# Performance work log

Measured on AMD Instinct MI355X. Metric: run time of the kernel, lower is better.

The kernel has to match this reference:

```python
import jax, jax.numpy as jnp
import numpy as np

T, NC, NT, D, H, LBL = 8, 512, 512, 256, 8, 3
NBF = 1419  # performer default: int(256 * ln(256))
EPS = 1e-4


def setup_inputs() -> dict:
    key = jax.random.key(0)
    ks = jax.random.split(key, 16)
    rn = lambda i, shape, sc=1.0: jax.random.normal(ks[i], shape, dtype=jnp.float32) * sc
    w = 1.0 / np.sqrt(D)
    return {
        'x_ctx': rn(0, (T, NC, D)),
        'label_train': rn(1, (T, NC, LBL)),
        'x_tgt': rn(2, (T, NT, D)),
        # task_encoder: 3-layer MLP (256+label_dim -> 256 -> 256 -> 256), ReLU
        'W1': rn(3, (D + LBL, D), 1.0 / np.sqrt(D + LBL)), 'b1': jnp.zeros((D,), jnp.float32),
        'W2': rn(4, (D, D), w), 'b2': jnp.zeros((D,), jnp.float32),
        'W3': rn(5, (D, D), w), 'b3': jnp.zeros((D,), jnp.float32),
        # per-head projections (8 distinct 256->256 Linears each for k/v/q)
        'Wk': rn(6, (H, D, D), w), 'bk': jnp.zeros((H, D), jnp.float32),
        'Wv': rn(7, (H, D, D), w), 'bv': jnp.zeros((H, D), jnp.float32),
        'Wq': rn(8, (H, D, D), w), 'bq': jnp.zeros((H, D), jnp.float32),
        # output head-merge projection (8*256 -> 256) and mu (256 -> 256)
        'Wo': rn(9, (H * D, D), 1.0 / np.sqrt(H * D)), 'bo': jnp.zeros((D,), jnp.float32),
        'Wmu': rn(10, (D, D), w), 'bmu': jnp.zeros((D,), jnp.float32),
        # FAVOR+ random projection matrix [nb_features, dim_head]
        'proj': rn(11, (NBF, D)),
    }


def _softmax_kernel(data, proj, is_query):
    # Performer FAVOR+ positive softmax-kernel features. data: [t,h,n,d]
    dn = D ** -0.25
    ratio = NBF ** -0.5
    dd = jnp.einsum('thnd,fd->thnf', data * dn, proj)          # [t,h,n,F]
    diag = 0.5 * jnp.sum(data * data, axis=-1) * (dn * dn)      # [t,h,n]
    if is_query:
        m = jnp.max(dd, axis=-1, keepdims=True)
    else:
        m = jnp.max(dd, axis=(-2, -1), keepdims=True)
    return ratio * (jnp.exp(dd - diag[..., None] - m) + EPS)


def reference(x_ctx, label_train, x_tgt, W1, b1, W2, b2, W3, b3,
              Wk, bk, Wv, bv, Wq, bq, Wo, bo, Wmu, bmu, proj):
    # task_encoder MLP on [x_ctx, label]
    h = jax.nn.relu(jnp.concatenate([x_ctx, label_train], axis=-1) @ W1 + b1)
    h = jax.nn.relu(h @ W2 + b2)
    cf = jax.nn.relu(h @ W3 + b3)                               # context_features [t,Nc,D]
    # per-head full-width projections: k from x_ctx, v from context_features, q from x_tgt
    k = jnp.einsum('tnd,hde->thne', x_ctx, Wk) + bk[None, :, None, :]
    v = jnp.einsum('tnd,hde->thne', cf, Wv) + bv[None, :, None, :]
    q = jnp.einsum('tnd,hde->thne', x_tgt, Wq) + bq[None, :, None, :]
    # non-causal Performer linear attention
    qp = _softmax_kernel(q, proj, True)                         # [t,h,Nt,F]
    kp = _softmax_kernel(k, proj, False)                        # [t,h,Nc,F]
    ksum = jnp.sum(kp, axis=-2)                                 # [t,h,F]
    d_inv = 1.0 / jnp.einsum('thnf,thf->thn', qp, ksum)         # [t,h,Nt]
    ctx = jnp.einsum('thnf,thne->thfe', kp, v)                  # [t,h,F,D]
    out = jnp.einsum('thnf,thfe,thn->thne', qp, ctx, d_inv)     # [t,h,Nt,D]
    # torch: permute(0,2,3,1).view(t,Nt,-1) -> head index fastest-varying
    out = jnp.transpose(out, (0, 2, 3, 1)).reshape(out.shape[0], out.shape[2], -1)
    rep = out @ Wo + bo                                         # [t,Nt,D]
    return rep @ Wmu + bmu                                      # mu / sample_features
```

## Files before the change

### kernel.cpp

```cpp
#include <hip/hip_runtime.h>
#include <hip/hip_bf16.h>

typedef __hip_bfloat16 bf16;
typedef __attribute__((ext_vector_type(8))) short short8;
typedef __attribute__((ext_vector_type(4))) float f32x4;
typedef __attribute__((ext_vector_type(4))) unsigned short us4;
#define DEV __device__ __forceinline__

static constexpr int T_ = 8, NC = 512, NT = 512, D_ = 256, H_ = 8, NBF = 1419;
static constexpr int FT32 = 46;
static constexpr float EPS_ = 1e-4f;
static constexpr float DN = 0.25f;
static constexpr float DIAG_SC = 0.03125f;

DEV float bf2f(unsigned short u) { return __uint_as_float(((unsigned)u) << 16); }
DEV float tofloat(bf16 x) { return __bfloat162float(x); }
DEV unsigned short f2bu(float x) { bf16 h = __float2bfloat16(x); return *(unsigned short*)&h; }

DEV float ldx(const void* p, long i, int isb) {
  if (isb) return bf2f(((const unsigned short*)p)[i]);
  return ((const float*)p)[i];
}
DEV void stx(void* p, long i, float v, int isb) {
  if (isb) ((bf16*)p)[i] = __float2bfloat16(v);
  else     ((float*)p)[i] = v;
}

DEV void async_copy16(const void* g, void* lds) {
  __builtin_amdgcn_global_load_lds(
      (const __attribute__((address_space(1))) unsigned int*)g,
      (__attribute__((address_space(3))) unsigned int*)lds, 16, 0, 0);
}

__global__ __launch_bounds__(256)
void detect_dtype(const void* __restrict__ x, int* __restrict__ flag)
{
  __shared__ int bad;
  if (threadIdx.x == 0) bad = 0;
  __syncthreads();
  int mybad = 0;
  for (int j = 0; j < 16; j++) {
    long i = 2L * (threadIdx.x + 256L * j);
    unsigned short u = ((const unsigned short*)x)[i];
    int e = (u >> 7) & 0xff, mant = u & 0x7f;
    bool b = (e == 0xff) || (e >= 141) || (e <= 93 && !(e == 0 && mant == 0));
    mybad += b ? 1 : 0;
  }
  atomicAdd(&bad, mybad);
  __syncthreads();
  if (threadIdx.x == 0) *flag = (bad > 1024) ? 0 : 1;
}

__global__ __launch_bounds__(256)
void conv_bf16(const void* __restrict__ src, bf16* __restrict__ dst,
               const int* __restrict__ dtFlag)
{
  const int fl = *dtFlag;
  long i = (long)blockIdx.x * 256 + threadIdx.x;
  dst[i] = __float2bfloat16(ldx(src, i, fl));
}

__global__ __launch_bounds__(256)
void prep_all(const void* __restrict__ Wk, const void* __restrict__ Wv,
              const void* __restrict__ Wq, const void* __restrict__ Wo,
              const void* __restrict__ W1, const void* __restrict__ W2,
              const void* __restrict__ W3, const void* __restrict__ Wmu,
              const void* __restrict__ proj, const void* __restrict__ x_ctx,
              bf16* __restrict__ WkT, bf16* __restrict__ WvT,
              bf16* __restrict__ WqT, bf16* __restrict__ WoT,
              bf16* __restrict__ W1T, bf16* __restrict__ W2T,
              bf16* __restrict__ W3T, bf16* __restrict__ WmuT,
              bf16* __restrict__ projB, bf16* __restrict__ xcB,
              float* __restrict__ zbase, const int* __restrict__ dtFlag)
{
  __shared__ float tile[32][33];
  const int fl = *dtFlag;
  const int kt = blockIdx.x, nt = blockIdx.y, z = blockIdx.z, t = threadIdx.x;

  if (z == 29) {
    int b = nt * 64 + kt;
#pragma unroll
    for (int r = 0; r < 3; r++) {
      int f = b * 3 + r;
      if (f < FT32 * 32) {
        float v = (f < NBF) ? ldx(proj, (long)f * 256 + t, fl) : 0.f;
        projB[(long)f * 256 + t] = __float2bfloat16(v);
      }
    }
    return;
  }
  if (z == 30) {
    int b = nt * 64 + kt;
#pragma unroll
    for (int j = 0; j < 8; j++) {
      long i = (long)b * 2048 + j * 256 + t;
      xcB[i] = __float2bfloat16(ldx(x_ctx, i, fl));
    }
    if (b < 320) zbase[b * 256 + t] = 0.f;
    return;
  }

  const void* in; bf16* out; int K; int perm = 0; long off = 0;
  if (z < 8)        { in = Wk;  out = WkT;  K = 256; off = (long)z * 65536; }
  else if (z < 16)  { in = Wv;  out = WvT;  K = 256; off = (long)(z - 8) * 65536; }
  else if (z < 24)  { in = Wq;  out = WqT;  K = 256; off = (long)(z - 16) * 65536; }
  else if (z == 24) { in = Wo;  out = WoT;  K = 2048; perm = 1; }
  else if (z == 25) { in = W1;  out = W1T;  K = 256; }
  else if (z == 26) { in = W2;  out = W2T;  K = 256; }
  else if (z == 27) { in = W3;  out = W3T;  K = 256; }
  else              { in = Wmu; out = WmuT; K = 256; }
  if (K == 256 && kt >= 8) return;
  const int k0 = kt * 32, n0 = nt * 32;
  const int row = t >> 3, cb = (t & 7) * 4;
  {
    int kk = k0 + row;
    int krow = perm ? (((kk & 255) << 3) | (kk >> 8)) : kk;
#pragma unroll
    for (int j = 0; j < 4; j++)
      tile[row][cb + j] = ldx(in, off + (long)krow * 256 + n0 + cb + j, fl);
  }
  __syncthreads();
  us4 o;
#pragma unroll
  for (int j = 0; j < 4; j++) o[j] = f2bu(tile[cb + j][row]);
  *(us4*)(out + off + (long)(n0 + row) * K + k0 + cb) = o;
}

__global__ __launch_bounds__(256)
void gemm_mfma(const bf16* __restrict__ A, const bf16* __restrict__ BT,
               const void* __restrict__ bias,
               void* __restrict__ C, int cMode, int epi, int cT,
               const int* __restrict__ dtFlag, float* __restrict__ diagOut,
               float* __restrict__ svOut,
               int M, int N, int K, long sA, int divA, long sB, int modB, long sBias)
{
  __shared__ alignas(16) bf16 As[2][64 * 64];
  __shared__ alignas(16) bf16 Bs[2][64 * 64];
  const int fl = *dtFlag;
  const int cB = (cMode == 2) ? fl : cMode;
  const int t = threadIdx.x;
  const int bz = blockIdx.z;
  const long aOff = (long)(bz / divA) * sA;
  const long bOff = (long)(bz % modB) * sB;
  const long biasOff = (long)(bz % modB) * sBias;
  const long cOff = (long)bz * (long)M * N;
  const int m0 = blockIdx.y * 64, n0 = blockIdx.x * 64;
  const int w = t >> 6, l = t & 63, quad = l >> 4, ln = l & 15;
  const bf16* Ab = A + aOff + (long)m0 * K;
  const bf16* Bb = BT + bOff + (long)n0 * K;
  const int srow = l >> 3;
  const int scc = (l & 7) ^ srow;
  f32x4 acc[4] = {};

  auto stage = [&](int buf, int k0) {
#pragma unroll
    for (int j = 0; j < 2; j++) {
      const int rbase = 32 * j + 8 * w;
      const int row = rbase + srow;
      async_copy16(Ab + (long)row * K + k0 + scc * 8, &As[buf][rbase * 64]);
      async_copy16(Bb + (long)row * K + k0 + scc * 8, &Bs[buf][rbase * 64]);
    }
  };

  stage(0, 0);
  __syncthreads();

  int cur = 0;
  for (int k0 = 0; k0 < K; k0 += 64) {
    if (k0 + 64 < K) stage(cur ^ 1, k0 + 64);
    const bf16* Ac = &As[cur][0];
    const bf16* Bc = &Bs[cur][0];
    const int arow = 16 * w + ln;
#pragma unroll
    for (int ks = 0; ks < 2; ks++) {
      short8 a = *(const short8*)(Ac + arow * 64 + (((ks * 4 + quad) ^ (arow & 7)) << 3));
#pragma unroll
      for (int i = 0; i < 4; i++) {
        const int brow = 16 * i + ln;
        short8 b = *(const short8*)(Bc + brow * 64 + (((ks * 4 + quad) ^ (brow & 7)) << 3));
        acc[i] = __builtin_amdgcn_mfma_f32_16x16x32_bf16(a, b, acc[i], 0, 0, 0);
      }
    }
    asm volatile("s_waitcnt vmcnt(0)" ::: "memory");
    __builtin_amdgcn_s_barrier();
    __builtin_amdgcn_sched_barrier(0);
    cur ^= 1;
  }

  float s2[4] = {0.f, 0.f, 0.f, 0.f};
  if (cT == 2) {
    const int mm = m0 + 16 * w + quad * 4;
    const int tile = mm >> 5, off = mm & 31;
#pragma unroll
    for (int i = 0; i < 4; i++) {
      int n = n0 + 16 * i + ln;
      us4 cv;
      float colsum = 0.f;
#pragma unroll
      for (int r = 0; r < 4; r++) {
        float c = acc[i][r];
        if (epi >= 1) c += ldx(bias, biasOff + n, fl);
        if (epi == 2) c = fmaxf(c, 0.f);
        colsum += c;
        cv[r] = f2bu(c);
      }
      *(us4*)((bf16*)C + cOff + ((long)tile * N + n) * 32 + off) = cv;
      if (svOut) {
        colsum += __shfl_xor(colsum, 16);
        colsum += __shfl_xor(colsum, 32);
        if (quad == 0) atomicAdd(&svOut[(long)bz * N + n], colsum);
      }
    }
  } else {
#pragma unroll
    for (int i = 0; i < 4; i++) {
#pragma unroll
      for (int r = 0; r < 4; r++) {
        int m = m0 + 16 * w + quad * 4 + r;
        int n = n0 + 16 * i + ln;
        float c = acc[i][r];
        if (epi >= 1) c += ldx(bias, biasOff + n, fl);
        if (epi == 2) c = fmaxf(c, 0.f);
        s2[r] += c * c;
        stx(C, cOff + (long)m * N + n, c, cB);
      }
    }
  }
  if (diagOut) {
#pragma unroll
    for (int r = 0; r < 4; r++) {
      float s = s2[r];
      s += __shfl_xor(s, 1); s += __shfl_xor(s, 2);
      s += __shfl_xor(s, 4); s += __shfl_xor(s, 8);
      if (ln == 0)
        atomicAdd(&diagOut[(long)bz * M + m0 + 16 * w + quad * 4 + r], DIAG_SC * s);
    }
  }
}

__global__ __launch_bounds__(256)
void gemm_mfma32v2(const bf16* __restrict__ A, const bf16* __restrict__ BT,
                   const void* __restrict__ bias,
                   void* __restrict__ C, int cMode, int epi,
                   const int* __restrict__ dtFlag, int M, int N, int K,
                   const void* __restrict__ labp, const void* __restrict__ labW)
{
  __shared__ alignas(16) bf16 As[2][32 * 64];
  __shared__ alignas(16) bf16 Bs[2][64 * 64];
  const int fl = *dtFlag;
  const int cB = (cMode == 2) ? fl : cMode;
  const int t = threadIdx.x;
  const int m0 = blockIdx.y * 32, n0 = blockIdx.x * 64;
  const int w = t >> 6, l = t & 63, quad = l >> 4, ln = l & 15;
  const int mi = w & 1, nh = w >> 1;
  const bf16* Ab = A + (long)m0 * K;
  const bf16* Bb = BT + (long)n0 * K;
  const int srow = l >> 3;
  const int scc = (l & 7) ^ srow;
  f32x4 acc[2] = {};

  auto stage = [&](int buf, int k0) {
    async_copy16(Ab + (long)(8 * w + srow) * K + k0 + scc * 8, &As[buf][(8 * w) * 64]);
#pragma unroll
    for (int j = 0; j < 2; j++) {
      const int rbase = 32 * j + 8 * w;
      async_copy16(Bb + (long)(rbase + srow) * K + k0 + scc * 8, &Bs[buf][rbase * 64]);
    }
  };

  stage(0, 0);
  __syncthreads();

  int cur = 0;
  for (int k0 = 0; k0 < K; k0 += 64) {
    if (k0 + 64 < K) stage(cur ^ 1, k0 + 64);
    const bf16* Ac = &As[cur][0];
    const bf16* Bc = &Bs[cur][0];
    const int arow = 16 * mi + ln;
#pragma unroll
    for (int ks = 0; ks < 2; ks++) {
      short8 a = *(const short8*)(Ac + arow * 64 + (((ks * 4 + quad) ^ (arow & 7)) << 3));
#pragma unroll
      for (int i = 0; i < 2; i++) {
        const int brow = 16 * (2 * nh + i) + ln;
        short8 b = *(const short8*)(Bc + brow * 64 + (((ks * 4 + quad) ^ (brow & 7)) << 3));
        acc[i] = __builtin_amdgcn_mfma_f32_16x16x32_bf16(a, b, acc[i], 0, 0, 0);
      }
    }
    asm volatile("s_waitcnt vmcnt(0)" ::: "memory");
    __builtin_amdgcn_s_barrier();
    __builtin_amdgcn_sched_barrier(0);
    cur ^= 1;
  }

#pragma unroll
  for (int i = 0; i < 2; i++) {
#pragma unroll
    for (int r = 0; r < 4; r++) {
      int m = m0 + 16 * mi + quad * 4 + r;
      int n = n0 + 16 * (2 * nh + i) + ln;
      float c = acc[i][r];
      if (epi >= 1) c += ldx(bias, n, fl);
      if (labp) {
#pragma unroll
        for (int j = 0; j < 3; j++)
          c += ldx(labp, (long)m * 3 + j, fl) * ldx(labW, (long)(256 + j) * 256 + n, fl);
      }
      if (epi == 2) c = fmaxf(c, 0.f);
      stx(C, (long)m * N + n, c, cB);
    }
  }
}

__global__ __launch_bounds__(256)
void key_fused_mfma(const bf16* __restrict__ k, const bf16* __restrict__ vQ,
                    const bf16* __restrict__ projB, const float* __restrict__ diagk,
                    float* __restrict__ ksumE, bf16* __restrict__ ctxQ,
                    float* __restrict__ mpart, float* __restrict__ csRp,
                    float* __restrict__ ktotp)
{
  __shared__ alignas(16) bf16 kS[3][32 * 256];
  __shared__ alignas(16) bf16 pS[2][64 * 40];
  __shared__ float wredM[4];
  __shared__ float wredK[4];

  const int bz = blockIdx.x, ft = blockIdx.y, f0 = ft * 64;
  const int t = threadIdx.x;
  const int w = t >> 6, l = t & 63, quad = l >> 4, ln = l & 15;
  const int fmine = f0 + 16 * w + ln;
  const bool fv = fmine < NBF;

  const bf16* kb = k + (long)bz * NC * 256;
  const bf16* vqb = vQ + (long)bz * 16 * 256 * 32;
  const float* db = diagk + bz * NC;

  auto stage = [&](int buf, int n0) {
#pragma unroll
    for (int j = 0; j < 4; j++) {
      int row = w * 8 + j * 2 + (l >> 5);
      int cc = (l & 31) ^ ((2 * j + (l >> 5)) & 7);
      async_copy16(kb + (long)(n0 + row) * 256 + cc * 8,
                   &kS[buf][w * 2048 + j * 512]);
    }
  };
  stage(0, 0);
  stage(1, 32);

  short8 pf[8];
  {
    const bf16* prow = projB + (long)fmine * 256;
#pragma unroll
    for (int kc = 0; kc < 8; kc++)
      pf[kc] = *(const short8*)(prow + kc * 32 + quad * 8);
  }

  f32x4 acc[4][4] = {};
  float ksumP = 0.f, mP = -1e30f;

  __syncthreads();

  int cur = 0;
  for (int it = 0; it < 16; it++) {
    const int n0 = it * 32;
    short8 bfr[4];
#pragma unroll
    for (int ei = 0; ei < 4; ei++) {
      int e = 64 * w + 16 * ei + ln;
      bfr[ei] = *(const short8*)(vqb + ((long)it * 256 + e) * 32 + quad * 8);
    }
    f32x4 dv0 = *(const f32x4*)(db + n0 + quad * 4);
    f32x4 dv1 = *(const f32x4*)(db + n0 + 16 + quad * 4);
    __builtin_amdgcn_sched_barrier(0);
    if (it + 2 < 16) {
      int nb = cur + 2; if (nb >= 3) nb -= 3;
      stage(nb, n0 + 64);
    }
    __builtin_amdgcn_sched_barrier(0);

    const bf16* kcur = &kS[cur][0];
    f32x4 dd[2][2] = {};
    __builtin_amdgcn_s_setprio(1);
#pragma unroll
    for (int kc = 0; kc < 8; kc++) {
      const int hf = kc & 1;
#pragma unroll
      for (int mi = 0; mi < 2; mi++) {
        short8 a = *(const short8*)(kcur + (16 * mi + ln) * 256 +
                                    (((kc * 4 + quad) ^ (ln & 7)) << 3));
        dd[mi][hf] = __builtin_amdgcn_mfma_f32_16x16x32_bf16(a, pf[kc], dd[mi][hf], 0, 0, 0);
      }
    }
    __builtin_amdgcn_s_setprio(0);
    bf16* pcur = &pS[it & 1][0];
#pragma unroll
    for (int mi = 0; mi < 2; mi++) {
      us4 ev;
      f32x4 dvv = mi ? dv1 : dv0;
#pragma unroll
      for (int r = 0; r < 4; r++) {
        float sc = DN * (dd[mi][0][r] + dd[mi][1][r]);
        float E = fv ? __expf(fminf(sc - dvv[r], 80.f)) : 0.f;
        unsigned short u = f2bu(E);
        ksumP += bf2f(u);
        if (fv) mP = fmaxf(mP, sc);
        ev[r] = u;
      }
      *(us4*)(pcur + (16 * w + ln) * 40 + 16 * mi + quad * 4) = ev;
    }
    asm volatile("s_waitcnt vmcnt(4) lgkmcnt(0)" ::: "memory");
    __builtin_amdgcn_s_barrier();
    __builtin_amdgcn_sched_barrier(0);

    __builtin_amdgcn_s_setprio(1);
#pragma unroll
    for (int fh = 0; fh < 4; fh++) {
      short8 a = *(const short8*)(pcur + (16 * fh + ln) * 40 + quad * 8);
#pragma unroll
      for (int ei = 0; ei < 4; ei++)
        acc[fh][ei] = __builtin_amdgcn_mfma_f32_16x16x32_bf16(a, bfr[ei], acc[fh][ei], 0, 0, 0);
    }
    __builtin_amdgcn_s_setprio(0);
    cur = (cur == 2) ? 0 : cur + 1;
  }
  __syncthreads();

#pragma unroll
  for (int fh = 0; fh < 4; fh++) {
    const int ft32 = 2 * ft + (fh >> 1);
    const int f32b = 16 * (fh & 1) + quad * 4;
#pragma unroll
    for (int ei = 0; ei < 4; ei++) {
      int e = 64 * w + 16 * ei + ln;
      us4 cv;
#pragma unroll
      for (int r = 0; r < 4; r++) cv[r] = f2bu(acc[fh][ei][r]);
      *(us4*)(&ctxQ[((long)(bz * FT32 + ft32) * 256 + e) * 32 + f32b]) = cv;
    }
  }

#pragma unroll
  for (int ei = 0; ei < 4; ei++) {
    float col = 0.f;
#pragma unroll
    for (int fh = 0; fh < 4; fh++)
#pragma unroll
      for (int r = 0; r < 4; r++) col += acc[fh][ei][r];
    col += __shfl_xor(col, 16);
    col += __shfl_xor(col, 32);
    if (quad == 0)
      csRp[((long)bz * 23 + ft) * 256 + 64 * w + 16 * ei + ln] = col;
  }

  float s = ksumP;
  s += __shfl_xor(s, 16); s += __shfl_xor(s, 32);
  if (quad == 0 && fv) ksumE[(long)bz * NBF + fmine] = s;
  float s2 = s;
  s2 += __shfl_xor(s2, 1); s2 += __shfl_xor(s2, 2);
  s2 += __shfl_xor(s2, 4); s2 += __shfl_xor(s2, 8);
  if (l == 0) wredK[w] = s2;

  float m = mP;
#pragma unroll
  for (int off = 1; off < 64; off <<= 1) m = fmaxf(m, __shfl_xor(m, off));
  if (l == 0) wredM[w] = m;
  __syncthreads();
  if (t == 0) {
    mpart[bz * 23 + ft] = fmaxf(fmaxf(wredM[0], wredM[1]), fmaxf(wredM[2], wredM[3]));
    ktotp[bz * 23 + ft] = wredK[0] + wredK[1] + wredK[2] + wredK[3];
  }
}

__global__ __launch_bounds__(256)
void finalize_red(const float* __restrict__ mpart, const float* __restrict__ csRp,
                  const float* __restrict__ ktotp, float* __restrict__ mk,
                  float* __restrict__ csR, float* __restrict__ ktotR)
{
  int bz = blockIdx.x, t = threadIdx.x;
  float s = 0.f;
  for (int ft = 0; ft < 23; ft++)
    s += csRp[((long)bz * 23 + ft) * 256 + t];
  csR[bz * 256 + t] = s;
  int w = t >> 6, l = t & 63;
  if (w == 0) {
    float m = (l < 23) ? mpart[bz * 23 + l] : -1e30f;
#pragma unroll
    for (int off = 32; off > 0; off >>= 1) m = fmaxf(m, __shfl_down(m, off));
    if (l == 0) mk[bz] = m;
  } else if (w == 1) {
    float kk = (l < 23) ? ktotp[bz * 23 + l] : 0.f;
#pragma unroll
    for (int off = 32; off > 0; off >>= 1) kk += __shfl_down(kk, off);
    if (l == 0) ktotR[bz] = kk;
  }
}

__global__ __launch_bounds__(256)
void q_fused_mfma(const bf16* __restrict__ xtB, const bf16* __restrict__ WqT,
                  const void* __restrict__ bq, const bf16* __restrict__ projB,
                  const bf16* __restrict__ ctxQ,
                  const float* __restrict__ ksum, const float* __restrict__ Sv,
                  const float* __restrict__ csR, const float* __restrict__ ktotR,
                  const float* __restrict__ mk, const int* __restrict__ dtFlag,
                  bf16* __restrict__ merged)
{
  __shared__ alignas(16) bf16 projS[3][32 * 256];
  __shared__ alignas(16) bf16 eS[2][64 * 40];
  __shared__ float dS[64];
  __shared__ float svS[256];
  __shared__ float crS[256];
  __shared__ float sS[64];
  __shared__ float mS[64];
  __shared__ float seS[64];

  const int fl = *dtFlag;
  const int bz = blockIdx.x, nt = blockIdx.y, t = threadIdx.x;
  const int w = t >> 6, l = t & 63, quad = l >> 4, ln = l & 15;
  const int tq = bz / H_, hh = bz % H_;
  const bf16* cqb = ctxQ + (long)bz * FT32 * 256 * 32;
  const float emk = __expf(-mk[bz]);
  const int srow = l >> 3, scc = (l & 7) ^ srow;

  bf16* scr = &projS[0][0];
  bf16* Asq = scr;
  bf16* Bsq = scr + 4096;
  const bf16* xq = xtB + ((long)tq * NT + nt * 64) * 256;
  const bf16* wq = WqT + (long)hh * 65536;
  f32x4 qacc[16] = {};

  for (int k0 = 0; k0 < 256; k0 += 64) {
#pragma unroll
    for (int j = 0; j < 2; j++) {
      const int rbase = 16 * w + 8 * j;
      async_copy16(xq + (long)(rbase + srow) * 256 + k0 + scc * 8, Asq + rbase * 64);
    }
#pragma unroll
    for (int j = 0; j < 8; j++) {
      const int rbase = 64 * w + 8 * j;
      async_copy16(wq + (long)(rbase + srow) * 256 + k0 + scc * 8, Bsq + rbase * 64);
    }
    asm volatile("s_waitcnt vmcnt(0)" ::: "memory");
    __builtin_amdgcn_s_barrier();
    __builtin_amdgcn_sched_barrier(0);
    const int arow = 16 * w + ln;
#pragma unroll
    for (int ks = 0; ks < 2; ks++) {
      short8 a = *(const short8*)(Asq + arow * 64 + (((ks * 4 + quad) ^ (arow & 7)) << 3));
#pragma unroll
      for (int g = 0; g < 16; g++) {
        const int brow = 16 * g + ln;
        short8 b = *(const short8*)(Bsq + brow * 64 + (((ks * 4 + quad) ^ (brow & 7)) << 3));
        qacc[g] = __builtin_amdgcn_mfma_f32_16x16x32_bf16(a, b, qacc[g], 0, 0, 0);
      }
    }
    __syncthreads();
  }
  {
    float sum2[4] = {0.f, 0.f, 0.f, 0.f};
#pragma unroll
    for (int g = 0; g < 16; g++) {
      float bias = ldx(bq, (long)hh * 256 + 16 * g + ln, fl);
#pragma unroll
      for (int r = 0; r < 4; r++) {
        float v = qacc[g][r] + bias;
        sum2[r] += v * v;
        scr[(16 * w + quad * 4 + r) * 264 + 16 * g + ln] = __float2bfloat16(v);
      }
    }
#pragma unroll
    for (int r = 0; r < 4; r++) {
      float s = sum2[r];
      s += __shfl_xor(s, 1); s += __shfl_xor(s, 2);
      s += __shfl_xor(s, 4); s += __shfl_xor(s, 8);
      if (ln == 0) dS[16 * w + quad * 4 + r] = DIAG_SC * s;
    }
  }
  asm volatile("s_waitcnt lgkmcnt(0)" ::: "memory");
  __builtin_amdgcn_sched_barrier(0);
  short8 qf[8];
#pragma unroll
  for (int kc = 0; kc < 8; kc++)
    qf[kc] = *(const short8*)(scr + (16 * w + ln) * 264 + kc * 32 + quad * 8);
  __syncthreads();

  auto stage_proj = [&](int buf, int f0n) {
#pragma unroll
    for (int j = 0; j < 4; j++) {
      int row = 8 * w + 2 * j + (l >> 5);
      int cc = (l & 31) ^ (row & 7);
      async_copy16(projB + (long)(f0n + row) * 256 + cc * 8,
                   &projS[buf][(8 * w + 2 * j) * 256]);
    }
  };
  stage_proj(0, 0);
  stage_proj(1, 32);
  svS[t] = Sv[bz * 256 + t];
  crS[t] = csR[bz * 256 + t];

  f32x4 acc[4][4] = {};
  float sPart[4] = {0.f, 0.f, 0.f, 0.f};
  float sEp[4] = {0.f, 0.f, 0.f, 0.f};
  float mPart[4] = {0.f, 0.f, 0.f, 0.f};
  __syncthreads();

  int cur = 0;
  for (int ft = 0; ft < FT32; ft++) {
    const int f0 = ft * 32;
    const bf16* pcur = &projS[cur][0];
    short8 cfr[4];
#pragma unroll
    for (int i = 0; i < 4; i++) {
      int e = 16 * (4 * w + i) + ln;
      cfr[i] = *(const short8*)(cqb + ((long)ft * 256 + e) * 32 + quad * 8);
    }
    const float kv0 = (f0 + ln < NBF) ? ksum[(long)bz * NBF + f0 + ln] : 0.f;
    const float kv1 = (f0 + 16 + ln < NBF) ? ksum[(long)bz * NBF + f0 + 16 + ln] : 0.f;
    __builtin_amdgcn_sched_barrier(0);
    if (ft + 2 < FT32) {
      int nb = cur + 2; if (nb >= 3) nb -= 3;
      stage_proj(nb, f0 + 64);
    }
    __builtin_amdgcn_sched_barrier(0);

    f32x4 dd0 = {}, dd1 = {};
    __builtin_amdgcn_s_setprio(1);
#pragma unroll
    for (int kc = 0; kc < 8; kc++) {
      const int co = ((kc * 4 + quad) ^ (ln & 7)) << 3;
      short8 b0 = *(const short8*)(pcur + ln * 256 + co);
      dd0 = __builtin_amdgcn_mfma_f32_16x16x32_bf16(qf[kc], b0, dd0, 0, 0, 0);
      short8 b1 = *(const short8*)(pcur + (16 + ln) * 256 + co);
      dd1 = __builtin_amdgcn_mfma_f32_16x16x32_bf16(qf[kc], b1, dd1, 0, 0, 0);
    }
    __builtin_amdgcn_s_setprio(0);
    const bool fv0 = (f0 + ln) < NBF;
    const bool fv1 = (f0 + 16 + ln) < NBF;
    bf16* ecur = &eS[ft & 1][0];
#pragma unroll
    for (int r = 0; r < 4; r++) {
      float E0 = fv0 ? __expf(fminf(DN * dd0[r], 80.f)) : 0.f;
      float E1 = fv1 ? __expf(fminf(DN * dd1[r], 80.f)) : 0.f;
      bf16 h0 = __float2bfloat16(E0), h1v = __float2bfloat16(E1);
      float e0 = tofloat(h0), e1 = tofloat(h1v);
      ecur[(16 * w + quad * 4 + r) * 40 + ln] = h0;
      ecur[(16 * w + quad * 4 + r) * 40 + 16 + ln] = h1v;
      sPart[r] += e0 * kv0 + e1 * kv1;
      sEp[r] += e0 + e1;
      mPart[r] = fmaxf(mPart[r], fmaxf(e0, e1));
    }
    asm volatile("s_waitcnt vmcnt(4) lgkmcnt(0)" ::: "memory");
    __builtin_amdgcn_s_barrier();
    __builtin_amdgcn_sched_barrier(0);

    __builtin_amdgcn_s_setprio(1);
#pragma unroll
    for (int mh = 0; mh < 4; mh++) {
      short8 a = *(const short8*)(ecur + (16 * mh + ln) * 40 + quad * 8);
#pragma unroll
      for (int i = 0; i < 4; i++)
        acc[mh][i] = __builtin_amdgcn_mfma_f32_16x16x32_bf16(a, cfr[i], acc[mh][i], 0, 0, 0);
    }
    __builtin_amdgcn_s_setprio(0);
    cur = (cur == 2) ? 0 : cur + 1;
  }
  __syncthreads();

#pragma unroll
  for (int r = 0; r < 4; r++) {
    float s = sPart[r], m = mPart[r], se = sEp[r];
#pragma unroll
    for (int off = 1; off < 16; off <<= 1) {
      s += __shfl_xor(s, off);
      m = fmaxf(m, __shfl_xor(m, off));
      se += __shfl_xor(se, off);
    }
    if (ln == 0) {
      sS[16 * w + quad * 4 + r] = s;
      mS[16 * w + quad * 4 + r] = m;
      seS[16 * w + quad * 4 + r] = se;
    }
  }
  __syncthreads();

  const float ktotv = ktotR[bz];
#pragma unroll
  for (int mh = 0; mh < 4; mh++) {
#pragma unroll
    for (int r = 0; r < 4; r++) {
      int row = 16 * mh + quad * 4 + r;
      float st = sS[row];
      float se = seS[row];
      float mt = fmaxf(mS[row], 1e-30f);
      float c = __expf(-dS[row]) / mt;
      float A = c * se + (float)NBF * EPS_;
      float den = emk * (c * st + EPS_ * ktotv) + (float)NC * EPS_ * A;
      float inv = 1.f / den;
#pragma unroll
      for (int i = 0; i < 4; i++) {
        int e = 16 * (4 * w + i) + ln;
        float val = (emk * (c * acc[mh][i][r] + EPS_ * crS[e]) + EPS_ * svS[e] * A) * inv;
        merged[((long)tq * NT + nt * 64 + row) * 2048 + hh * 256 + e] =
            __float2bfloat16(val);
      }
    }
  }
}

extern "C" void kernel_launch(void* const* d_in, const int* in_sizes, int n_in,
                              void* d_out, int out_size, void* d_ws, size_t ws_size,
                              hipStream_t stream)
{
  const void* x_ctx = d_in[0];
  const void* label = d_in[1];
  const void* x_tgt = d_in[2];
  const void* W1 = d_in[3];
  const void* b1 = d_in[4];
  const void* W2 = d_in[5];
  const void* b2 = d_in[6];
  const void* W3 = d_in[7];
  const void* b3 = d_in[8];
  const void* Wk = d_in[9];
  const void* bk = d_in[10];
  const void* Wv = d_in[11];
  const void* bv = d_in[12];
  const void* Wq = d_in[13];
  const void* bq = d_in[14];
  const void* Wo = d_in[15];
  const void* bo = d_in[16];
  const void* Wmu = d_in[17];
  const void* bmu = d_in[18];
  const void* proj = d_in[19];

  float* W = (float*)d_ws;
  const long F0 = 0, F1 = 4194304, F2 = 8388608;
  const long CTXQ_F = (long)64 * FT32 * 256 * 32 / 2;
  const long F3 = F2 + CTXQ_F;
  bf16* kB = (bf16*)(W + F0);
  bf16* xtB = (bf16*)(W + F0);
  bf16* rep = (bf16*)(W + F0 + 1048576);
  bf16* vQ = (bf16*)(W + F1);
  bf16* merged = (bf16*)(W + F1);
  bf16* h1 = (bf16*)(W + F2);
  bf16* h2 = (bf16*)(W + F2 + 524288);
  bf16* cf = (bf16*)(W + F2 + 1048576);
  bf16* xcB = (bf16*)(W + F2 + 1572864);
  bf16* ctxQ = (bf16*)(W + F2);
  long o = F3;
  auto alloc = [&](long n) { float* p = W + o; o += n; return p; };
  float* zbase = W + o;
  float* dgk = alloc(32768);
  float* dgq = alloc(32768);
  float* Sv = alloc(64 * 256);
  float* csR = alloc(64 * 256);
  float* ktotR = alloc(64);
  alloc(192);
  float* ksumE = alloc((long)64 * NBF);
  float* mpart = alloc(64 * 23);
  float* mk = alloc(64);
  int* dtFlag = (int*)alloc(64);
  float* csRp = alloc((long)64 * 23 * 256);
  float* ktotp = alloc(64 * 23);
  bf16* projB = (bf16*)alloc((long)FT32 * 32 * 256 / 2);
  bf16* WkT = (bf16*)alloc(262144);
  bf16* WvT = (bf16*)alloc(262144);
  bf16* WqT = (bf16*)alloc(262144);
  bf16* WoT = (bf16*)alloc(262144);
  bf16* W1T = (bf16*)alloc(32768);
  bf16* W2T = (bf16*)alloc(32768);
  bf16* W3T = (bf16*)alloc(32768);
  bf16* WmuT = (bf16*)alloc(32768);
  (void)ws_size; (void)in_sizes; (void)n_in; (void)out_size; (void)dgq;

  const dim3 B(256);
  detect_dtype<<<1, B, 0, stream>>>(x_ctx, dtFlag);
  prep_all<<<dim3(64, 8, 31), B, 0, stream>>>(
      Wk, Wv, Wq, Wo, W1, W2, W3, Wmu, proj, x_ctx,
      WkT, WvT, WqT, WoT, W1T, W2T, W3T, WmuT, projB, xcB, zbase, dtFlag);
  gemm_mfma32v2<<<dim3(4, 128), B, 0, stream>>>(
      xcB, W1T, b1, h1, 1, 2, dtFlag, 4096, 256, 256, label, W1);
  gemm_mfma32v2<<<dim3(4, 128), B, 0, stream>>>(
      h1, W2T, b2, h2, 1, 2, dtFlag, 4096, 256, 256, nullptr, nullptr);
  gemm_mfma32v2<<<dim3(4, 128), B, 0, stream>>>(
      h2, W3T, b3, cf, 1, 2, dtFlag, 4096, 256, 256, nullptr, nullptr);
  gemm_mfma<<<dim3(4, 8, 64), B, 0, stream>>>(
      xcB, WkT, bk, kB, 1, 1, 0, dtFlag, dgk, nullptr,
      512, 256, 256, 131072L, 8, 65536L, 8, 256L);
  gemm_mfma<<<dim3(4, 8, 64), B, 0, stream>>>(
      cf, WvT, bv, vQ, 1, 1, 2, dtFlag, nullptr, Sv,
      512, 256, 256, 131072L, 8, 65536L, 8, 256L);
  key_fused_mfma<<<dim3(64, 23), B, 0, stream>>>(kB, vQ, projB, dgk, ksumE, ctxQ,
                                                 mpart, csRp, ktotp);
  finalize_red<<<64, B, 0, stream>>>(mpart, csRp, ktotp, mk, csR, ktotR);
  conv_bf16<<<4096, B, 0, stream>>>(x_tgt, xtB, dtFlag);
  q_fused_mfma<<<dim3(64, 8), B, 0, stream>>>(xtB, WqT, bq, projB, ctxQ, ksumE,
                                              Sv, csR, ktotR, mk, dtFlag, merged);
  gemm_mfma32v2<<<dim3(4, 128), B, 0, stream>>>(
      merged, WoT, bo, rep, 1, 1, dtFlag, 4096, 256, 2048, nullptr, nullptr);
  gemm_mfma32v2<<<dim3(4, 128), B, 0, stream>>>(
      rep, WmuT, bmu, d_out, 2, 1, dtFlag, 4096, 256, 256, nullptr, nullptr);
}
```

Before: 368.5 us.

## Fold x_tgt conversion and finalize reduction into neighbors; triple-buffer gemm

Moves the x_tgt bf16 conversion into the prep_all kernel as an extra z-slice, giving xtB its own workspace buffer. It also drops the finalize_red kernel by having q_fused_mfma reduce the per-tile partials directly. The small GEMM moves from double to triple buffering with a partial vmcnt wait, and the last iterations of the fused kernels now drain with vmcnt(0). The aim is fewer kernel launches and better load/compute overlap, at the cost of redundant reductions across the 8 q blocks per head and more LDS in the GEMM.

```diff
diff --git a/kernel.cpp b/kernel.cpp
--- a/kernel.cpp
+++ b/kernel.cpp
@@ -52,25 +52,18 @@
 }
 
 __global__ __launch_bounds__(256)
-void conv_bf16(const void* __restrict__ src, bf16* __restrict__ dst,
-               const int* __restrict__ dtFlag)
-{
-  const int fl = *dtFlag;
-  long i = (long)blockIdx.x * 256 + threadIdx.x;
-  dst[i] = __float2bfloat16(ldx(src, i, fl));
-}
-
-__global__ __launch_bounds__(256)
 void prep_all(const void* __restrict__ Wk, const void* __restrict__ Wv,
               const void* __restrict__ Wq, const void* __restrict__ Wo,
               const void* __restrict__ W1, const void* __restrict__ W2,
               const void* __restrict__ W3, const void* __restrict__ Wmu,
               const void* __restrict__ proj, const void* __restrict__ x_ctx,
+              const void* __restrict__ x_tgt,
               bf16* __restrict__ WkT, bf16* __restrict__ WvT,
               bf16* __restrict__ WqT, bf16* __restrict__ WoT,
               bf16* __restrict__ W1T, bf16* __restrict__ W2T,
               bf16* __restrict__ W3T, bf16* __restrict__ WmuT,
               bf16* __restrict__ projB, bf16* __restrict__ xcB,
+              bf16* __restrict__ xtB,
               float* __restrict__ zbase, const int* __restrict__ dtFlag)
 {
   __shared__ float tile[32][33];
@@ -97,6 +90,15 @@
       xcB[i] = __float2bfloat16(ldx(x_ctx, i, fl));
     }
     if (b < 320) zbase[b * 256 + t] = 0.f;
+    return;
+  }
+  if (z == 31) {
+    int b = nt * 64 + kt;
+#pragma unroll
+    for (int j = 0; j < 8; j++) {
+      long i = (long)b * 2048 + j * 256 + t;
+      xtB[i] = __float2bfloat16(ldx(x_tgt, i, fl));
+    }
     return;
   }
 
@@ -245,8 +247,8 @@
                    const int* __restrict__ dtFlag, int M, int N, int K,
                    const void* __restrict__ labp, const void* __restrict__ labW)
 {
-  __shared__ alignas(16) bf16 As[2][32 * 64];
-  __shared__ alignas(16) bf16 Bs[2][64 * 64];
+  __shared__ alignas(16) bf16 As[3][32 * 64];
+  __shared__ alignas(16) bf16 Bs[3][64 * 64];
   const int fl = *dtFlag;
   const int cB = (cMode == 2) ? fl : cMode;
   const int t = threadIdx.x;
@@ -257,6 +259,7 @@
   const bf16* Bb = BT + (long)n0 * K;
   const int srow = l >> 3;
   const int scc = (l & 7) ^ srow;
+  const int niter = K >> 6;
   f32x4 acc[2] = {};
 
   auto stage = [&](int buf, int k0) {
@@ -269,11 +272,16 @@
   };
 
   stage(0, 0);
+  if (niter > 1) stage(1, 64);
   __syncthreads();
 
   int cur = 0;
-  for (int k0 = 0; k0 < K; k0 += 64) {
-    if (k0 + 64 < K) stage(cur ^ 1, k0 + 64);
+  for (int it = 0; it < niter; ++it) {
+    if (it + 2 < niter) {
+      int nb = cur + 2; if (nb >= 3) nb -= 3;
+      stage(nb, (it + 2) * 64);
+    }
+    __builtin_amdgcn_sched_barrier(0);
     const bf16* Ac = &As[cur][0];
     const bf16* Bc = &Bs[cur][0];
     const int arow = 16 * mi + ln;
@@ -287,10 +295,14 @@
         acc[i] = __builtin_amdgcn_mfma_f32_16x16x32_bf16(a, b, acc[i], 0, 0, 0);
       }
     }
-    asm volatile("s_waitcnt vmcnt(0)" ::: "memory");
+    if (it + 2 < niter) {
+      asm volatile("s_waitcnt vmcnt(3)" ::: "memory");
+    } else {
+      asm volatile("s_waitcnt vmcnt(0)" ::: "memory");
+    }
     __builtin_amdgcn_s_barrier();
     __builtin_amdgcn_sched_barrier(0);
-    cur ^= 1;
+    cur = (cur == 2) ? 0 : cur + 1;
   }
 
 #pragma unroll
@@ -407,7 +419,11 @@
       }
       *(us4*)(pcur + (16 * w + ln) * 40 + 16 * mi + quad * 4) = ev;
     }
-    asm volatile("s_waitcnt vmcnt(4) lgkmcnt(0)" ::: "memory");
+    if (it + 2 < 16) {
+      asm volatile("s_waitcnt vmcnt(4) lgkmcnt(0)" ::: "memory");
+    } else {
+      asm volatile("s_waitcnt vmcnt(0) lgkmcnt(0)" ::: "memory");
+    }
     __builtin_amdgcn_s_barrier();
     __builtin_amdgcn_sched_barrier(0);
 
@@ -471,36 +487,12 @@
 }
 
 __global__ __launch_bounds__(256)
-void finalize_red(const float* __restrict__ mpart, const float* __restrict__ csRp,
-                  const float* __restrict__ ktotp, float* __restrict__ mk,
-                  float* __restrict__ csR, float* __restrict__ ktotR)
-{
-  int bz = blockIdx.x, t = threadIdx.x;
-  float s = 0.f;
-  for (int ft = 0; ft < 23; ft++)
-    s += csRp[((long)bz * 23 + ft) * 256 + t];
-  csR[bz * 256 + t] = s;
-  int w = t >> 6, l = t & 63;
-  if (w == 0) {
-    float m = (l < 23) ? mpart[bz * 23 + l] : -1e30f;
-#pragma unroll
-    for (int off = 32; off > 0; off >>= 1) m = fmaxf(m, __shfl_down(m, off));
-    if (l == 0) mk[bz] = m;
-  } else if (w == 1) {
-    float kk = (l < 23) ? ktotp[bz * 23 + l] : 0.f;
-#pragma unroll
-    for (int off = 32; off > 0; off >>= 1) kk += __shfl_down(kk, off);
-    if (l == 0) ktotR[bz] = kk;
-  }
-}
-
-__global__ __launch_bounds__(256)
 void q_fused_mfma(const bf16* __restrict__ xtB, const bf16* __restrict__ WqT,
                   const void* __restrict__ bq, const bf16* __restrict__ projB,
                   const bf16* __restrict__ ctxQ,
                   const float* __restrict__ ksum, const float* __restrict__ Sv,
-                  const float* __restrict__ csR, const float* __restrict__ ktotR,
-                  const float* __restrict__ mk, const int* __restrict__ dtFlag,
+                  const float* __restrict__ csRp, const float* __restrict__ ktotp,
+                  const float* __restrict__ mpart, const int* __restrict__ dtFlag,
                   bf16* __restrict__ merged)
 {
   __shared__ alignas(16) bf16 projS[3][32 * 256];
@@ -517,8 +509,20 @@
   const int w = t >> 6, l = t & 63, quad = l >> 4, ln = l & 15;
   const int tq = bz / H_, hh = bz % H_;
   const bf16* cqb = ctxQ + (long)bz * FT32 * 256 * 32;
-  const float emk = __expf(-mk[bz]);
   const int srow = l >> 3, scc = (l & 7) ^ srow;
+
+  float mkv = -1e30f, ktv = 0.f;
+  {
+    float s = 0.f;
+    for (int f2 = 0; f2 < 23; f2++) {
+      s += csRp[((long)bz * 23 + f2) * 256 + t];
+      mkv = fmaxf(mkv, mpart[bz * 23 + f2]);
+      ktv += ktotp[bz * 23 + f2];
+    }
+    crS[t] = s;
+  }
+  const float emk = __expf(-mkv);
+  const float ktotv = ktv;
 
   bf16* scr = &projS[0][0];
   bf16* Asq = scr;
@@ -594,7 +598,6 @@
   stage_proj(0, 0);
   stage_proj(1, 32);
   svS[t] = Sv[bz * 256 + t];
-  crS[t] = csR[bz * 256 + t];
 
   f32x4 acc[4][4] = {};
   float sPart[4] = {0.f, 0.f, 0.f, 0.f};
@@ -647,7 +650,11 @@
       sEp[r] += e0 + e1;
       mPart[r] = fmaxf(mPart[r], fmaxf(e0, e1));
     }
-    asm volatile("s_waitcnt vmcnt(4) lgkmcnt(0)" ::: "memory");
+    if (ft + 2 < FT32) {
+      asm volatile("s_waitcnt vmcnt(4) lgkmcnt(0)" ::: "memory");
+    } else {
+      asm volatile("s_waitcnt vmcnt(0) lgkmcnt(0)" ::: "memory");
+    }
     __builtin_amdgcn_s_barrier();
     __builtin_amdgcn_sched_barrier(0);
 
@@ -681,7 +688,6 @@
   }
   __syncthreads();
 
-  const float ktotv = ktotR[bz];
 #pragma unroll
   for (int mh = 0; mh < 4; mh++) {
 #pragma unroll
@@ -735,7 +741,6 @@
   const long CTXQ_F = (long)64 * FT32 * 256 * 32 / 2;
   const long F3 = F2 + CTXQ_F;
   bf16* kB = (bf16*)(W + F0);
-  bf16* xtB = (bf16*)(W + F0);
   bf16* rep = (bf16*)(W + F0 + 1048576);
   bf16* vQ = (bf16*)(W + F1);
   bf16* merged = (bf16*)(W + F1);
@@ -760,6 +765,7 @@
   float* csRp = alloc((long)64 * 23 * 256);
   float* ktotp = alloc(64 * 23);
   bf16* projB = (bf16*)alloc((long)FT32 * 32 * 256 / 2);
+  bf16* xtB = (bf16*)alloc(524288);
   bf16* WkT = (bf16*)alloc(262144);
   bf16* WvT = (bf16*)alloc(262144);
   bf16* WqT = (bf16*)alloc(262144);
@@ -768,13 +774,14 @@
   bf16* W2T = (bf16*)alloc(32768);
   bf16* W3T = (bf16*)alloc(32768);
   bf16* WmuT = (bf16*)alloc(32768);
-  (void)ws_size; (void)in_sizes; (void)n_in; (void)out_size; (void)dgq;
+  (void)ws_size; (void)in_sizes; (void)n_in; (void)out_size;
+  (void)dgq; (void)csR; (void)ktotR; (void)mk;
 
   const dim3 B(256);
   detect_dtype<<<1, B, 0, stream>>>(x_ctx, dtFlag);
-  prep_all<<<dim3(64, 8, 31), B, 0, stream>>>(
-      Wk, Wv, Wq, Wo, W1, W2, W3, Wmu, proj, x_ctx,
-      WkT, WvT, WqT, WoT, W1T, W2T, W3T, WmuT, projB, xcB, zbase, dtFlag);
+  prep_all<<<dim3(64, 8, 32), B, 0, stream>>>(
+      Wk, Wv, Wq, Wo, W1, W2, W3, Wmu, proj, x_ctx, x_tgt,
+      WkT, WvT, WqT, WoT, W1T, W2T, W3T, WmuT, projB, xcB, xtB, zbase, dtFlag);
   gemm_mfma32v2<<<dim3(4, 128), B, 0, stream>>>(
       xcB, W1T, b1, h1, 1, 2, dtFlag, 4096, 256, 256, label, W1);
   gemm_mfma32v2<<<dim3(4, 128), B, 0, stream>>>(
@@ -789,10 +796,8 @@
       512, 256, 256, 131072L, 8, 65536L, 8, 256L);
   key_fused_mfma<<<dim3(64, 23), B, 0, stream>>>(kB, vQ, projB, dgk, ksumE, ctxQ,
                                                  mpart, csRp, ktotp);
-  finalize_red<<<64, B, 0, stream>>>(mpart, csRp, ktotp, mk, csR, ktotR);
-  conv_bf16<<<4096, B, 0, stream>>>(x_tgt, xtB, dtFlag);
   q_fused_mfma<<<dim3(64, 8), B, 0, stream>>>(xtB, WqT, bq, projB, ctxQ, ksumE,
-                                              Sv, csR, ktotR, mk, dtFlag, merged);
+                                              Sv, csRp, ktotp, mpart, dtFlag, merged);
   gemm_mfma32v2<<<dim3(4, 128), B, 0, stream>>>(
       merged, WoT, bo, rep, 1, 1, dtFlag, 4096, 256, 2048, nullptr, nullptr);
   gemm_mfma32v2<<<dim3(4, 128), B, 0, stream>>>(
```

After: 359.6 us (median of 2 runs). -2.4%, faster.
